# Kernel optimization log

Hardware: AMD Instinct MI355X
Metric: run time of the kernel (lower is better)

The kernel has to match this reference:

```python
import jax, jax.numpy as jnp
import numpy as np

L, H, NH, NKV, HD, I, V, B, S = 18, 640, 4, 1, 256, 2048, 32768, 1, 1024
WINDOW = 512
EPS = 1e-6
THETA_G = 1000000.0
THETA_L = 10000.0


def _rms(x, w):
    # Gemma RMSNorm: x / rms(x) * (1 + w)
    var = jnp.mean(jnp.square(x), axis=-1, keepdims=True)
    return x * jax.lax.rsqrt(var + EPS) * (1.0 + w)


def _rope_tables(theta):
    inv = 1.0 / (theta ** (jnp.arange(0, HD, 2, dtype=jnp.float32) / HD))
    f = jnp.arange(S, dtype=jnp.float32)[:, None] * inv[None, :]
    emb = jnp.concatenate([f, f], axis=-1)  # [S, HD]
    return jnp.cos(emb), jnp.sin(emb)


def _rope(x, cos, sin):
    # x: [B, S, n, HD]
    x1, x2 = jnp.split(x, 2, axis=-1)
    rot = jnp.concatenate([-x2, x1], axis=-1)
    return x * cos[None, :, None, :] + rot * sin[None, :, None, :]


def setup_inputs() -> dict:
    key = jax.random.key(0)
    ks = jax.random.split(key, 16)
    r = lambda k, sh: jax.random.normal(k, sh, jnp.float32) * 0.02
    return {
        'input_ids': jax.random.randint(ks[0], (B, S), 0, V, jnp.int32),
        'is_full': jnp.array([(i + 1) % 6 == 0 for i in range(L)]),
        'embed': r(ks[1], (V, H)),
        'wq': r(ks[2], (L, H, NH * HD)),
        'wk': r(ks[3], (L, H, NKV * HD)),
        'wv': r(ks[4], (L, H, NKV * HD)),
        'wo': r(ks[5], (L, NH * HD, H)),
        'qn': jnp.zeros((L, HD)), 'kn': jnp.zeros((L, HD)),
        'ln1': jnp.zeros((L, H)), 'ln2': jnp.zeros((L, H)),
        'ln3': jnp.zeros((L, H)), 'ln4': jnp.zeros((L, H)),
        'wg': r(ks[6], (L, H, I)), 'wu': r(ks[7], (L, H, I)),
        'wd': r(ks[8], (L, I, H)),
        'norm_w': jnp.zeros((H,)),
    }


def _forward(embed, wq, wk, wv, wo, qn, kn, ln1, ln2, ln3, ln4, wg, wu, wd,
             norm_w, input_ids, is_full):
    cos_g, sin_g = _rope_tables(THETA_G)
    cos_l, sin_l = _rope_tables(THETA_L)
    pos = jnp.arange(S)
    causal = pos[:, None] >= pos[None, :]
    sliding = causal & ((pos[:, None] - pos[None, :]) < WINDOW)
    scale = HD ** -0.5
    grp = NH // NKV

    h = embed[input_ids] * jnp.asarray(H ** 0.5, embed.dtype)  # [B,S,H]

    def body(h, xs):
        (wq_, wk_, wv_, wo_, qn_, kn_, l1, l2, l3, l4, wg_, wu_, wd_, full) = xs
        cos = jnp.where(full, cos_g, cos_l)
        sin = jnp.where(full, sin_g, sin_l)
        mask = jnp.where(full, causal, sliding)
        x = _rms(h, l1)
        q = (x @ wq_).reshape(B, S, NH, HD)
        k = (x @ wk_).reshape(B, S, NKV, HD)
        v = (x @ wv_).reshape(B, S, NKV, HD)
        q = _rope(_rms(q, qn_), cos, sin)
        k = _rope(_rms(k, kn_), cos, sin)
        qg = q.reshape(B, S, NKV, grp, HD)
        scores = jnp.einsum('bqngd,bsnd->bngqs', qg, k) * scale
        scores = jnp.where(mask[None, None, None], scores, -1e30)
        attn = jax.nn.softmax(scores, axis=-1)
        o = jnp.einsum('bngqs,bsnd->bqngd', attn, v).reshape(B, S, NH * HD)
        h = h + _rms(o @ wo_, l2)               # post_attention_layernorm then residual
        x = _rms(h, l3)                          # pre_feedforward_layernorm
        mlp = (jax.nn.gelu(x @ wg_, approximate=True) * (x @ wu_)) @ wd_  # GeGLU
        h = h + _rms(mlp, l4)                    # post_feedforward_layernorm then residual
        return h, None

    h, _ = jax.lax.scan(body, h, (wq, wk, wv, wo, qn, kn, ln1, ln2, ln3, ln4, wg, wu, wd, is_full))
    h = _rms(h, norm_w)
    # lm_head tied to embed_tokens; final_logit_softcapping = 0.0 (disabled)
    return jnp.einsum('bsh,vh->bsv', h, embed)


def reference(input_ids, is_full, embed, wq, wk, wv, wo, qn, kn,
              ln1, ln2, ln3, ln4, wg, wu, wd, norm_w):
    return _forward(embed, wq, wk, wv, wo, qn, kn, ln1, ln2, ln3, ln4,
                    wg, wu, wd, norm_w, input_ids, is_full)
```

## Files before the change

### kernel.cpp

```cpp
#include <hip/hip_runtime.h>


typedef unsigned short u16;
typedef __attribute__((ext_vector_type(4))) float f32x4;
typedef __attribute__((ext_vector_type(8))) short bf16x8;

#define DEV static __device__ __forceinline__
#define BIGN (1 << 30)

DEV u16 f2bf(float f) {
  union { float f; unsigned u; } x; x.f = f;
  unsigned r = x.u + 0x7fffu + ((x.u >> 16) & 1u);
  return (u16)(r >> 16);
}

#define GLOAD16(gp, lp) __builtin_amdgcn_global_load_lds( \
    (const __attribute__((address_space(1))) void*)(gp), \
    (__attribute__((address_space(3))) void*)(lp), 16, 0, 0)

DEV float blockSum(float v, float* red) {
#pragma unroll
  for (int o = 32; o; o >>= 1) v += __shfl_down(v, o);
  int lane = threadIdx.x & 63, wid = threadIdx.x >> 6;
  if (lane == 0) red[wid] = v;
  __syncthreads();
  float s = red[0] + red[1] + red[2] + red[3];
  __syncthreads();
  return s;
}

DEV float blockMax(float v, float* red) {
#pragma unroll
  for (int o = 32; o; o >>= 1) v = fmaxf(v, __shfl_down(v, o));
  int lane = threadIdx.x & 63, wid = threadIdx.x >> 6;
  if (lane == 0) red[wid] = v;
  __syncthreads();
  float s = fmaxf(fmaxf(red[0], red[1]), fmaxf(red[2], red[3]));
  __syncthreads();
  return s;
}

DEV void cstore(float* C, size_t i, float v) { C[i] = v; }
DEV void cstore(u16* C, size_t i, float v) { C[i] = f2bf(v); }

template <typename CT, int GEGLU, int BMODE>
__global__ __launch_bounds__(256) void gemm_nt(
    const u16* __restrict__ A, int lda, long sA,
    const void* __restrict__ B0v, int ldb0,
    const void* __restrict__ B1v, int ldb1,
    const void* __restrict__ B2v, int ldb2,
    int ns1, int ns2,
    CT* __restrict__ C, int ldc, long sC,
    int K, float alpha, int kmode, int nshift, int ksplit) {
  __shared__ __align__(16) u16 As[2 * 128 * 64];
  __shared__ __align__(16) u16 Bs[2 * 128 * 64];
  const int m0 = blockIdx.y * 128;
  int n0;
  if (nshift == -1) n0 = blockIdx.x * 128;
  else if (nshift == -2) { n0 = blockIdx.x * 128; if (n0 > m0) return; }
  else { n0 = m0 - nshift + blockIdx.x * 128; if (n0 < 0) return; }
  int klo = 0, khi = K;
  if (kmode == 1) { klo = m0 - 512; if (klo < 0) klo = 0; khi = m0 + 128; if (khi > K) khi = K; }
  else if (kmode == 2) { khi = m0 + 128; if (khi > K) khi = K; }
  else if (kmode == 3) { int kl = K / ksplit; klo = blockIdx.z * kl; khi = klo + kl; }
  A += (long)blockIdx.z * sA;

  const int t = threadIdx.x;
  const int l = t & 63, w = t >> 6;
  const int wr = w >> 1, wc = w & 1;
  const int lr = l & 15, lk = l >> 4;
  const int axr = lr & 7;
  const int srow = t >> 3;
  const int scolx = ((t & 7) ^ (srow & 7)) << 3;
  const u16* Ag = A + (size_t)(m0 + srow) * lda + scolx;
  const int nsteps = (khi - klo) >> 6;

  auto stageA = [&](int db, int k0) {
    u16* al = As + db * 8192 + w * 512;
#pragma unroll
    for (int p = 0; p < 4; ++p)
      GLOAD16(Ag + k0 + (size_t)(32 * p) * lda, al + p * 2048);
  };

  const u16* Bg16 = nullptr;
  const float* Bp = nullptr; int bldb = 0, bcol = 0, krow0 = 0;
  f32x4 fb[8];
  if constexpr (BMODE == 0) {
    Bg16 = (const u16*)B0v + (size_t)(n0 + srow) * ldb0 + scolx;
  } else if constexpr (BMODE == 1) {
    int rv = n0 + (l & 31) * 4;
    if (GEGLU) {
      int half = (rv >> 4) & 1;
      Bp = (const float*)(half ? B1v : B0v);
      bldb = half ? ldb1 : ldb0;
      bcol = (rv >> 5) * 16 + (rv & 15);
    } else if (rv >= ns2) { Bp = (const float*)B2v; bldb = ldb2; bcol = rv - ns2; }
    else if (rv >= ns1)   { Bp = (const float*)B1v; bldb = ldb1; bcol = rv - ns1; }
    else                  { Bp = (const float*)B0v; bldb = ldb0; bcol = rv; }
    krow0 = w * 16 + (l >> 5) * 8;
  } else {
    Bp = (const float*)B0v;
  }

  auto stageB0 = [&](int db, int k0) {
    u16* bl = Bs + db * 8192 + w * 512;
#pragma unroll
    for (int p = 0; p < 4; ++p)
      GLOAD16(Bg16 + k0 + (size_t)(32 * p) * ldb0, bl + p * 2048);
  };
  auto loadB = [&](int k0) {
    if constexpr (BMODE == 1) {
#pragma unroll
      for (int j = 0; j < 8; ++j)
        fb[j] = *(const f32x4*)&Bp[(size_t)(k0 + krow0 + j) * bldb + bcol];
    } else if constexpr (BMODE == 2) {
#pragma unroll
      for (int p = 0; p < 4; ++p)
#pragma unroll
        for (int q = 0; q < 2; ++q)
          fb[p * 2 + q] = *(const f32x4*)&Bp[(size_t)(n0 + srow + 32 * p) * ldb0 +
                                             k0 + (((t & 7) ^ (srow & 7)) << 3) + q * 4];
    }
  };
  auto writeB = [&](int db) {
    if constexpr (BMODE == 1) {
      int kb = w * 2 + (l >> 5);
#pragma unroll
      for (int e = 0; e < 4; ++e) {
        int row = (l & 31) * 4 + e;
        u16 tmp[8];
#pragma unroll
        for (int j = 0; j < 8; ++j) tmp[j] = f2bf(fb[j][e]);
        *(int4*)&Bs[db * 8192 + row * 64 + ((kb ^ (row & 7)) << 3)] = *(int4*)tmp;
      }
    } else if constexpr (BMODE == 2) {
#pragma unroll
      for (int p = 0; p < 4; ++p) {
        u16 tmp[8];
#pragma unroll
        for (int j = 0; j < 8; ++j) tmp[j] = f2bf(fb[p * 2 + j / 4][j & 3]);
        *(int4*)&Bs[db * 8192 + (srow + 32 * p) * 64 + ((t & 7) << 3)] = *(int4*)tmp;
      }
    }
  };

  f32x4 acc[4][4] = {};
  auto compute = [&](int db) {
    const u16* Ab = As + db * 8192;
    const u16* Bb = Bs + db * 8192;
    bf16x8 af[2][4], bfr[2][4];
#pragma unroll
    for (int kk = 0; kk < 2; ++kk)
#pragma unroll
      for (int i = 0; i < 4; ++i) {
        af[kk][i]  = *(const bf16x8*)&Ab[(wr * 64 + i * 16 + lr) * 64 + (((kk * 4 + lk) ^ axr) << 3)];
        bfr[kk][i] = *(const bf16x8*)&Bb[(wc * 64 + i * 16 + lr) * 64 + (((kk * 4 + lk) ^ axr) << 3)];
      }
#pragma unroll
    for (int kk = 0; kk < 2; ++kk)
#pragma unroll
      for (int mi = 0; mi < 4; ++mi)
#pragma unroll
        for (int ni = 0; ni < 4; ++ni)
          acc[mi][ni] = __builtin_amdgcn_mfma_f32_16x16x32_bf16(af[kk][mi], bfr[kk][ni], acc[mi][ni], 0, 0, 0);
  };

  if constexpr (BMODE == 0) {
    stageA(0, klo); stageB0(0, klo);
    for (int s = 0; s < nsteps; ++s) {
      __syncthreads();
      const int db = s & 1;
      if (s + 1 < nsteps) { stageA(db ^ 1, klo + (s + 1) * 64); stageB0(db ^ 1, klo + (s + 1) * 64); }
      compute(db);
    }
  } else {
    loadB(klo); stageA(0, klo);
    for (int s = 0; s < nsteps; ++s) {
      const int db = s & 1;
      writeB(db);
      if (s + 1 < nsteps) loadB(klo + (s + 1) * 64);
      __syncthreads();
      if (s + 1 < nsteps) stageA(db ^ 1, klo + (s + 1) * 64);
      compute(db);
    }
  }

  C += (long)blockIdx.z * sC;
  if (GEGLU) {
#pragma unroll
    for (int mi = 0; mi < 4; ++mi) {
      int row = m0 + wr * 64 + mi * 16 + lk * 4;
#pragma unroll
      for (int np = 0; np < 2; ++np) {
        int col = (n0 + wc * 64) / 2 + np * 16 + lr;
#pragma unroll
        for (int j = 0; j < 4; ++j) {
          float g = acc[mi][2 * np][j], u = acc[mi][2 * np + 1][j];
          float z = 0.7978845608028654f * (g + 0.044715f * g * g * g);
          float th = 2.0f / (1.0f + __expf(-2.0f * z)) - 1.0f;
          cstore(C, (size_t)(row + j) * ldc + col, 0.5f * g * (1.0f + th) * u);
        }
      }
    }
  } else {
#pragma unroll
    for (int mi = 0; mi < 4; ++mi) {
      int row = m0 + wr * 64 + mi * 16 + lk * 4;
#pragma unroll
      for (int ni = 0; ni < 4; ++ni) {
        int col = n0 + wc * 64 + ni * 16 + lr;
#pragma unroll
        for (int j = 0; j < 4; ++j)
          cstore(C, (size_t)(row + j) * ldc + col, acc[mi][ni][j] * alpha);
      }
    }
  }
}

__global__ void gather_rms_kernel(const int* __restrict__ ids, const float* __restrict__ embed,
                                  const float* __restrict__ w, float* __restrict__ h,
                                  u16* __restrict__ x) {
  __shared__ float red[8];
  const int s = blockIdx.x, t = threadIdx.x;
  const float* src = embed + (size_t)ids[s] * 640;
  const float scale = sqrtf(640.0f);
  float hv[3];
  float ss = 0.0f;
#pragma unroll
  for (int i = 0; i < 3; ++i) {
    int c = t + i * 256;
    float v = (c < 640) ? src[c] * scale : 0.0f;
    hv[i] = v; ss += v * v;
  }
  ss = blockSum(ss, red);
  const float sc = rsqrtf(ss * (1.0f / 640.0f) + 1e-6f);
#pragma unroll
  for (int i = 0; i < 3; ++i) {
    int c = t + i * 256;
    if (c < 640) {
      h[(size_t)s * 640 + c] = hv[i];
      x[(size_t)s * 640 + c] = f2bf(hv[i] * sc * (1.0f + w[c]));
    }
  }
}

__global__ void fused_add_norm(float* __restrict__ h, const float* __restrict__ t1,
                               int nsl, const float* __restrict__ wa,
                               const float* __restrict__ wn, u16* __restrict__ xout) {
  __shared__ float red[8];
  const int row = blockIdx.x, t = threadIdx.x;
  float ts[3], hv[3];
  float ss = 0.0f;
#pragma unroll
  for (int i = 0; i < 3; ++i) {
    int c = t + i * 256;
    float v = 0.0f;
    if (c < 640) {
      v = t1[(size_t)row * 640 + c];
      for (int z = 1; z < nsl; ++z) v += t1[(size_t)z * 655360 + (size_t)row * 640 + c];
    }
    ts[i] = v; ss += v * v;
  }
  ss = blockSum(ss, red);
  const float s1 = rsqrtf(ss * (1.0f / 640.0f) + 1e-6f);
  float ss2 = 0.0f;
#pragma unroll
  for (int i = 0; i < 3; ++i) {
    int c = t + i * 256;
    float v = 0.0f;
    if (c < 640) v = h[(size_t)row * 640 + c] + ts[i] * s1 * (1.0f + wa[c]);
    hv[i] = v; ss2 += v * v;
  }
  ss2 = blockSum(ss2, red);
  const float s2 = rsqrtf(ss2 * (1.0f / 640.0f) + 1e-6f);
#pragma unroll
  for (int i = 0; i < 3; ++i) {
    int c = t + i * 256;
    if (c < 640) {
      h[(size_t)row * 640 + c] = hv[i];
      xout[(size_t)row * 640 + c] = f2bf(hv[i] * s2 * (1.0f + wn[c]));
    }
  }
}

__global__ void rope_tables_kernel(float* cg, float* sg, float* cl, float* sl) {
  int s = blockIdx.x, t = threadIdx.x;
  float e = -(float)t * (1.0f / 128.0f);
  float ag = (float)s * expf(e * logf(1000000.0f));
  float al = (float)s * expf(e * logf(10000.0f));
  cg[s * 128 + t] = cosf(ag); sg[s * 128 + t] = sinf(ag);
  cl[s * 128 + t] = cosf(al); sl[s * 128 + t] = sinf(al);
}

__global__ void rope_fused(const float* __restrict__ qkvf, const float* __restrict__ qn,
                           const float* __restrict__ kn, u16* __restrict__ qb,
                           u16* __restrict__ kb, u16* __restrict__ vt,
                           const float* __restrict__ ct, const float* __restrict__ st) {
  __shared__ float red[8];
  __shared__ float sh[256];
  const int s = blockIdx.x, hh = blockIdx.y, t = threadIdx.x;
  const long SL = (long)1024 * 1536;
  if (hh == 5) {
    long i = (size_t)s * 1536 + 1280 + t;
    vt[(size_t)t * 1024 + s] = f2bf(qkvf[i] + qkvf[i + SL]);
    return;
  }
  long i = (size_t)s * 1536 + hh * 256 + t;
  const float* nw = (hh == 4) ? kn : qn;
  float x = qkvf[i] + qkvf[i + SL];
  float ss = blockSum(x * x, red);
  float n = x * rsqrtf(ss * (1.0f / 256.0f) + 1e-6f) * (1.0f + nw[t]);
  sh[t] = n;
  __syncthreads();
  float cosv = ct[s * 128 + (t & 127)];
  float sinv = st[s * 128 + (t & 127)];
  float partner = (t < 128) ? -sh[t + 128] : sh[t - 128];
  u16 r = f2bf(n * cosv + partner * sinv);
  if (hh == 4) kb[(size_t)s * 256 + t] = r;
  else qb[((size_t)hh * 1024 + s) * 256 + t] = r;
}

__global__ void softmax_kernel(const float* __restrict__ sc, u16* __restrict__ P, int mode) {
  __shared__ float red[8];
  const int i = blockIdx.x, hh = blockIdx.y, t = threadIdx.x;
  const float* row = sc + ((size_t)hh * 1024 + i) * 1024;
  u16* prow = P + ((size_t)hh * 1024 + i) * 1024;
  const int m0 = i & ~127;
  int lo = 0, wlo = 0;
  if (mode) {
    lo = i - 511; if (lo < 0) lo = 0;
    wlo = m0 - 512; if (wlo < 0) wlo = 0;
  }
  const int whi = m0 + 127;
  float m = -1e30f;
  for (int j = lo + t; j <= i; j += 256) m = fmaxf(m, row[j]);
  m = blockMax(m, red);
  float sum = 0.0f;
  for (int j = lo + t; j <= i; j += 256) sum += __expf(row[j] - m);
  sum = blockSum(sum, red);
  float inv = 1.0f / sum;
  for (int j = wlo + t; j <= whi; j += 256) {
    float v = (j >= lo && j <= i) ? __expf(row[j] - m) * inv : 0.0f;
    prow[j] = f2bf(v);
  }
}

extern "C" void kernel_launch(void* const* d_in, const int* in_sizes, int n_in,
                              void* d_out, int out_size, void* d_ws, size_t ws_size,
                              hipStream_t stream) {
  (void)in_sizes; (void)n_in; (void)out_size; (void)ws_size;
  const int*   ids   = (const int*)d_in[0];
  const float* embed = (const float*)d_in[2];
  const float* wq    = (const float*)d_in[3];
  const float* wk    = (const float*)d_in[4];
  const float* wv    = (const float*)d_in[5];
  const float* wo    = (const float*)d_in[6];
  const float* qn    = (const float*)d_in[7];
  const float* kn    = (const float*)d_in[8];
  const float* ln1   = (const float*)d_in[9];
  const float* ln2   = (const float*)d_in[10];
  const float* ln3   = (const float*)d_in[11];
  const float* ln4   = (const float*)d_in[12];
  const float* wg    = (const float*)d_in[13];
  const float* wu    = (const float*)d_in[14];
  const float* wd    = (const float*)d_in[15];
  const float* nw    = (const float*)d_in[16];
  float* out = (float*)d_out;

  const int S = 1024, H = 640, NH = 4, HD = 256, I = 2048, V = 32768;

  unsigned char* p = (unsigned char*)d_ws;
  auto alloc = [&](size_t b) { void* r = (void*)p; p += (b + 255) & ~(size_t)255; return r; };
  float* h     = (float*)alloc((size_t)S * H * 4);
  u16*   x     = (u16*)alloc((size_t)S * H * 2);
  float* qkvf  = (float*)alloc((size_t)2 * S * 1536 * 4);
  u16*   qb    = (u16*)alloc((size_t)NH * S * HD * 2);
  u16*   kb    = (u16*)alloc((size_t)S * HD * 2);
  u16*   vt    = (u16*)alloc((size_t)HD * S * 2);
  float* scp   = (float*)alloc((size_t)NH * S * S * 4);
  u16*   P     = (u16*)alloc((size_t)NH * S * S * 2);
  u16*   o     = (u16*)alloc((size_t)S * NH * HD * 2);
  float* t1    = (float*)alloc((size_t)4 * S * H * 4);
  u16*   mg    = (u16*)alloc((size_t)S * I * 2);
  u16*   hn    = (u16*)alloc((size_t)S * H * 2);
  float* cg    = (float*)alloc((size_t)S * 128 * 4);
  float* sg    = (float*)alloc((size_t)S * 128 * 4);
  float* cl    = (float*)alloc((size_t)S * 128 * 4);
  float* sl2   = (float*)alloc((size_t)S * 128 * 4);

  rope_tables_kernel<<<S, 128, 0, stream>>>(cg, sg, cl, sl2);
  gather_rms_kernel<<<S, 256, 0, stream>>>(ids, embed, ln1, h, x);

  for (int l = 0; l < 18; ++l) {
    bool full = ((l + 1) % 6) == 0;
    const float* wq_l = wq + (size_t)l * H * 1024;
    const float* wk_l = wk + (size_t)l * H * 256;
    const float* wv_l = wv + (size_t)l * H * 256;
    const float* wo_l = wo + (size_t)l * 1024 * H;
    const float* wg_l = wg + (size_t)l * H * I;
    const float* wu_l = wu + (size_t)l * H * I;
    const float* wd_l = wd + (size_t)l * I * H;

    gemm_nt<float, 0, 1><<<dim3(12, 8, 2), 256, 0, stream>>>(
        x, H, 0, wq_l, 1024, wk_l, 256, wv_l, 256, 1024, 1280,
        qkvf, 1536, (long)S * 1536, H, 1.0f, 3, -1, 2);
    rope_fused<<<dim3(S, 6), 256, 0, stream>>>(qkvf, qn + l * HD, kn + l * HD, qb, kb, vt,
                                               full ? cg : cl, full ? sg : sl2);
    if (full)
      gemm_nt<float, 0, 0><<<dim3(8, 8, NH), 256, 0, stream>>>(
          qb, HD, (long)S * HD, kb, HD, nullptr, 0, nullptr, 0, BIGN, BIGN,
          scp, S, (long)S * S, HD, 0.0625f, 0, -2, 1);
    else
      gemm_nt<float, 0, 0><<<dim3(5, 8, NH), 256, 0, stream>>>(
          qb, HD, (long)S * HD, kb, HD, nullptr, 0, nullptr, 0, BIGN, BIGN,
          scp, S, (long)S * S, HD, 0.0625f, 0, 512, 1);
    softmax_kernel<<<dim3(S, NH), 256, 0, stream>>>(scp, P, full ? 0 : 1);
    gemm_nt<u16, 0, 0><<<dim3(2, 8, NH), 256, 0, stream>>>(
        P, S, (long)S * S, vt, S, nullptr, 0, nullptr, 0, BIGN, BIGN,
        o, NH * HD, HD, S, 1.0f, full ? 2 : 1, -1, 1);
    gemm_nt<float, 0, 1><<<dim3(5, 8, 2), 256, 0, stream>>>(
        o, NH * HD, 0, wo_l, 640, nullptr, 0, nullptr, 0, BIGN, BIGN,
        t1, H, (long)S * H, NH * HD, 1.0f, 3, -1, 2);
    fused_add_norm<<<S, 256, 0, stream>>>(h, t1, 2, ln2 + l * H, ln3 + l * H, x);

    gemm_nt<u16, 1, 1><<<dim3(32, 8, 1), 256, 0, stream>>>(
        x, H, 0, wg_l, 2048, wu_l, 2048, nullptr, 0, BIGN, BIGN,
        mg, I, 0, H, 1.0f, 0, -1, 1);
    gemm_nt<float, 0, 1><<<dim3(5, 8, 4), 256, 0, stream>>>(
        mg, I, 0, wd_l, 640, nullptr, 0, nullptr, 0, BIGN, BIGN,
        t1, H, (long)S * H, I, 1.0f, 3, -1, 4);
    fused_add_norm<<<S, 256, 0, stream>>>(h, t1, 4, ln4 + l * H,
                                          (l == 17) ? nw : ln1 + (l + 1) * H,
                                          (l == 17) ? hn : x);
  }

  gemm_nt<float, 0, 2><<<dim3(V / 128, 8, 1), 256, 0, stream>>>(
      hn, H, 0, embed, H, nullptr, 0, nullptr, 0, BIGN, BIGN,
      out, V, 0, H, 1.0f, 0, -1, 1);
}
```

Before: 2.187 ms.

## Fuse softmax into PV matmul and swizzle block order for GeGLU/lm_head GEMMs

Removes the separate softmax kernel and bf16 P buffer. A new pv_fused kernel computes each row's max and sum from the fp32 scores, then forms normalized probabilities on the fly while feeding MFMA against V staged in LDS. It also adds a 1D grid mapping (nshift -3) that groups 8x8 tiles of M x N blocks for better L2 reuse in the GeGLU and lm_head GEMMs. The fused kernel reads the fp32 scores twice and runs only 64 blocks with single-buffered V loads, which may limit occupancy.

```diff
diff --git a/kernel.cpp b/kernel.cpp
--- a/kernel.cpp
+++ b/kernel.cpp
@@ -25,17 +25,6 @@
   if (lane == 0) red[wid] = v;
   __syncthreads();
   float s = red[0] + red[1] + red[2] + red[3];
-  __syncthreads();
-  return s;
-}
-
-DEV float blockMax(float v, float* red) {
-#pragma unroll
-  for (int o = 32; o; o >>= 1) v = fmaxf(v, __shfl_down(v, o));
-  int lane = threadIdx.x & 63, wid = threadIdx.x >> 6;
-  if (lane == 0) red[wid] = v;
-  __syncthreads();
-  float s = fmaxf(fmaxf(red[0], red[1]), fmaxf(red[2], red[3]));
   __syncthreads();
   return s;
 }
@@ -54,11 +43,17 @@
     int K, float alpha, int kmode, int nshift, int ksplit) {
   __shared__ __align__(16) u16 As[2 * 128 * 64];
   __shared__ __align__(16) u16 Bs[2 * 128 * 64];
-  const int m0 = blockIdx.y * 128;
-  int n0;
-  if (nshift == -1) n0 = blockIdx.x * 128;
-  else if (nshift == -2) { n0 = blockIdx.x * 128; if (n0 > m0) return; }
-  else { n0 = m0 - nshift + blockIdx.x * 128; if (n0 < 0) return; }
+  int m0, n0;
+  if (nshift == -3) {
+    int b = blockIdx.x;
+    m0 = ((b >> 3) & 7) * 128;
+    n0 = ((b >> 6) * 8 + (b & 7)) * 128;
+  } else {
+    m0 = blockIdx.y * 128;
+    if (nshift == -1) n0 = blockIdx.x * 128;
+    else if (nshift == -2) { n0 = blockIdx.x * 128; if (n0 > m0) return; }
+    else { n0 = m0 - nshift + blockIdx.x * 128; if (n0 < 0) return; }
+  }
   int klo = 0, khi = K;
   if (kmode == 1) { klo = m0 - 512; if (klo < 0) klo = 0; khi = m0 + 128; if (khi > K) khi = K; }
   else if (kmode == 2) { khi = m0 + 128; if (khi > K) khi = K; }
@@ -217,6 +212,115 @@
   }
 }
 
+__global__ __launch_bounds__(256) void pv_fused(
+    const float* __restrict__ scp, const u16* __restrict__ vt,
+    u16* __restrict__ o, int isfull) {
+  __shared__ __align__(16) u16 Vs[256 * 64];
+  __shared__ float mrow[64], invl[64];
+  const int m0 = blockIdx.x * 64, z = blockIdx.y;
+  const float* S_ = scp + (size_t)z * 1024 * 1024;
+  const int t = threadIdx.x;
+
+  {
+    int r = t >> 2, q = t & 3;
+    int row = m0 + r;
+    int lo = isfull ? 0 : (row - 511 > 0 ? row - 511 : 0);
+    const float* rp = S_ + (size_t)row * 1024;
+    float mx = -1e30f;
+    for (int j = lo + q; j <= row; j += 4) mx = fmaxf(mx, rp[j]);
+    mx = fmaxf(mx, __shfl_xor(mx, 1));
+    mx = fmaxf(mx, __shfl_xor(mx, 2));
+    float sum = 0.0f;
+    for (int j = lo + q; j <= row; j += 4) sum += __expf(rp[j] - mx);
+    sum += __shfl_xor(sum, 1);
+    sum += __shfl_xor(sum, 2);
+    if (q == 0) { mrow[r] = mx; invl[r] = 1.0f / sum; }
+  }
+  __syncthreads();
+
+  const int l = t & 63, w = t >> 6;
+  const int wr = w >> 1, wc = w & 1;
+  const int lr = l & 15, lk = l >> 4;
+  const int axr = lr & 7;
+  const int srow = t >> 3;
+  const int scolx = ((t & 7) ^ (srow & 7)) << 3;
+  const u16* Bg = vt + (size_t)srow * 1024 + scolx;
+  const int klo = isfull ? 0 : (m0 - 512 > 0 ? m0 - 512 : 0);
+  const int nsteps = (m0 + 64 - klo) >> 6;
+
+  int rowi[2]; float ms[2], ls[2];
+#pragma unroll
+  for (int i = 0; i < 2; ++i) {
+    rowi[i] = wr * 32 + i * 16 + lr;
+    ms[i] = mrow[rowi[i]];
+    ls[i] = invl[rowi[i]];
+  }
+
+  f32x4 acc[2][8] = {};
+  for (int s = 0; s < nsteps; ++s) {
+    const int k0 = klo + s * 64;
+    if (s) __syncthreads();
+    {
+      u16* bl = Vs + w * 512;
+#pragma unroll
+      for (int p = 0; p < 8; ++p)
+        GLOAD16(Bg + k0 + (size_t)(32 * p) * 1024, bl + p * 2048);
+    }
+    bf16x8 af[2][2];
+#pragma unroll
+    for (int kk = 0; kk < 2; ++kk)
+#pragma unroll
+      for (int i = 0; i < 2; ++i) {
+        int row = m0 + rowi[i];
+        int kb = k0 + kk * 32 + lk * 8;
+        const float* ap = S_ + (size_t)row * 1024 + kb;
+        float4 v0 = *(const float4*)ap;
+        float4 v1 = *(const float4*)(ap + 4);
+        float vv[8] = {v0.x, v0.y, v0.z, v0.w, v1.x, v1.y, v1.z, v1.w};
+        int lo = isfull ? 0 : row - 511;
+        u16 tmp[8];
+#pragma unroll
+        for (int e = 0; e < 8; ++e) {
+          int k = kb + e;
+          float pv = __expf(vv[e] - ms[i]) * ls[i];
+          tmp[e] = f2bf((k >= lo && k <= row) ? pv : 0.0f);
+        }
+        af[kk][i] = *(bf16x8*)tmp;
+      }
+    __syncthreads();
+#pragma unroll
+    for (int kk = 0; kk < 2; ++kk)
+#pragma unroll
+      for (int nh = 0; nh < 2; ++nh) {
+        bf16x8 bfr[4];
+#pragma unroll
+        for (int i = 0; i < 4; ++i)
+          bfr[i] = *(const bf16x8*)&Vs[(nh * 128 + wc * 64 + i * 16 + lr) * 64 +
+                                       (((kk * 4 + lk) ^ axr) << 3)];
+#pragma unroll
+        for (int mi = 0; mi < 2; ++mi)
+#pragma unroll
+          for (int ni = 0; ni < 4; ++ni)
+            acc[mi][nh * 4 + ni] = __builtin_amdgcn_mfma_f32_16x16x32_bf16(
+                af[kk][mi], bfr[ni], acc[mi][nh * 4 + ni], 0, 0, 0);
+      }
+  }
+
+#pragma unroll
+  for (int mi = 0; mi < 2; ++mi) {
+    int row = m0 + wr * 32 + mi * 16 + lk * 4;
+#pragma unroll
+    for (int nh = 0; nh < 2; ++nh)
+#pragma unroll
+      for (int ni = 0; ni < 4; ++ni) {
+        int col = z * 256 + nh * 128 + wc * 64 + ni * 16 + lr;
+#pragma unroll
+        for (int j = 0; j < 4; ++j)
+          o[(size_t)(row + j) * 1024 + col] = f2bf(acc[mi][nh * 4 + ni][j]);
+      }
+  }
+}
+
 __global__ void gather_rms_kernel(const int* __restrict__ ids, const float* __restrict__ embed,
                                   const float* __restrict__ w, float* __restrict__ h,
                                   u16* __restrict__ x) {
@@ -318,31 +422,6 @@
   u16 r = f2bf(n * cosv + partner * sinv);
   if (hh == 4) kb[(size_t)s * 256 + t] = r;
   else qb[((size_t)hh * 1024 + s) * 256 + t] = r;
-}
-
-__global__ void softmax_kernel(const float* __restrict__ sc, u16* __restrict__ P, int mode) {
-  __shared__ float red[8];
-  const int i = blockIdx.x, hh = blockIdx.y, t = threadIdx.x;
-  const float* row = sc + ((size_t)hh * 1024 + i) * 1024;
-  u16* prow = P + ((size_t)hh * 1024 + i) * 1024;
-  const int m0 = i & ~127;
-  int lo = 0, wlo = 0;
-  if (mode) {
-    lo = i - 511; if (lo < 0) lo = 0;
-    wlo = m0 - 512; if (wlo < 0) wlo = 0;
-  }
-  const int whi = m0 + 127;
-  float m = -1e30f;
-  for (int j = lo + t; j <= i; j += 256) m = fmaxf(m, row[j]);
-  m = blockMax(m, red);
-  float sum = 0.0f;
-  for (int j = lo + t; j <= i; j += 256) sum += __expf(row[j] - m);
-  sum = blockSum(sum, red);
-  float inv = 1.0f / sum;
-  for (int j = wlo + t; j <= whi; j += 256) {
-    float v = (j >= lo && j <= i) ? __expf(row[j] - m) * inv : 0.0f;
-    prow[j] = f2bf(v);
-  }
 }
 
 extern "C" void kernel_launch(void* const* d_in, const int* in_sizes, int n_in,
@@ -378,7 +457,6 @@
   u16*   kb    = (u16*)alloc((size_t)S * HD * 2);
   u16*   vt    = (u16*)alloc((size_t)HD * S * 2);
   float* scp   = (float*)alloc((size_t)NH * S * S * 4);
-  u16*   P     = (u16*)alloc((size_t)NH * S * S * 2);
   u16*   o     = (u16*)alloc((size_t)S * NH * HD * 2);
   float* t1    = (float*)alloc((size_t)4 * S * H * 4);
   u16*   mg    = (u16*)alloc((size_t)S * I * 2);
@@ -414,18 +492,15 @@
       gemm_nt<float, 0, 0><<<dim3(5, 8, NH), 256, 0, stream>>>(
           qb, HD, (long)S * HD, kb, HD, nullptr, 0, nullptr, 0, BIGN, BIGN,
           scp, S, (long)S * S, HD, 0.0625f, 0, 512, 1);
-    softmax_kernel<<<dim3(S, NH), 256, 0, stream>>>(scp, P, full ? 0 : 1);
-    gemm_nt<u16, 0, 0><<<dim3(2, 8, NH), 256, 0, stream>>>(
-        P, S, (long)S * S, vt, S, nullptr, 0, nullptr, 0, BIGN, BIGN,
-        o, NH * HD, HD, S, 1.0f, full ? 2 : 1, -1, 1);
+    pv_fused<<<dim3(16, NH), 256, 0, stream>>>(scp, vt, o, full ? 1 : 0);
     gemm_nt<float, 0, 1><<<dim3(5, 8, 2), 256, 0, stream>>>(
         o, NH * HD, 0, wo_l, 640, nullptr, 0, nullptr, 0, BIGN, BIGN,
         t1, H, (long)S * H, NH * HD, 1.0f, 3, -1, 2);
     fused_add_norm<<<S, 256, 0, stream>>>(h, t1, 2, ln2 + l * H, ln3 + l * H, x);
 
-    gemm_nt<u16, 1, 1><<<dim3(32, 8, 1), 256, 0, stream>>>(
+    gemm_nt<u16, 1, 1><<<dim3(256, 1, 1), 256, 0, stream>>>(
         x, H, 0, wg_l, 2048, wu_l, 2048, nullptr, 0, BIGN, BIGN,
-        mg, I, 0, H, 1.0f, 0, -1, 1);
+        mg, I, 0, H, 1.0f, 0, -3, 1);
     gemm_nt<float, 0, 1><<<dim3(5, 8, 4), 256, 0, stream>>>(
         mg, I, 0, wd_l, 640, nullptr, 0, nullptr, 0, BIGN, BIGN,
         t1, H, (long)S * H, I, 1.0f, 3, -1, 4);
@@ -434,7 +509,7 @@
                                           (l == 17) ? hn : x);
   }
 
-  gemm_nt<float, 0, 2><<<dim3(V / 128, 8, 1), 256, 0, stream>>>(
+  gemm_nt<float, 0, 2><<<dim3(2048, 1, 1), 256, 0, stream>>>(
       hn, H, 0, embed, H, nullptr, 0, nullptr, 0, BIGN, BIGN,
-      out, V, 0, H, 1.0f, 0, -1, 1);
-}
+      out, V, 0, H, 1.0f, 0, -3, 1);
+}
```

After: 2.890 ms. 1.32x slower.

## Pre-convert embedding to bf16, drop split-K on QKV, read V directly from projection

Applied to the files above, without the earlier changes.

The tied embedding is converted to bf16 once up front, so the LM-head GEMM can use async LDS loads (BMODE 0) instead of converting fp32 per tile. That GEMM also gets a swizzled 1D block mapping that groups blocks sharing embedding columns. The QKV projection drops split-K, which removes the partial-sum buffer and the add in rope. The separate V-transpose pass is removed, and the PV GEMM reads V in fp32 straight from the QKV buffer through the k-major convert path. The trade-offs are lower QKV parallelism, an extra conversion pass over the embedding, and fp32 V reads repeated for each head.

```diff
diff --git a/kernel.cpp b/kernel.cpp
--- a/kernel.cpp
+++ b/kernel.cpp
@@ -54,11 +54,17 @@
     int K, float alpha, int kmode, int nshift, int ksplit) {
   __shared__ __align__(16) u16 As[2 * 128 * 64];
   __shared__ __align__(16) u16 Bs[2 * 128 * 64];
-  const int m0 = blockIdx.y * 128;
-  int n0;
-  if (nshift == -1) n0 = blockIdx.x * 128;
-  else if (nshift == -2) { n0 = blockIdx.x * 128; if (n0 > m0) return; }
-  else { n0 = m0 - nshift + blockIdx.x * 128; if (n0 < 0) return; }
+  int m0, n0;
+  if (nshift == -3) {
+    int b = blockIdx.x;
+    m0 = ((b >> 3) & 7) * 128;
+    n0 = ((b >> 6) * 8 + (b & 7)) * 128;
+  } else {
+    m0 = blockIdx.y * 128;
+    if (nshift == -1) n0 = blockIdx.x * 128;
+    else if (nshift == -2) { n0 = blockIdx.x * 128; if (n0 > m0) return; }
+    else { n0 = m0 - nshift + blockIdx.x * 128; if (n0 < 0) return; }
+  }
   int klo = 0, khi = K;
   if (kmode == 1) { klo = m0 - 512; if (klo < 0) klo = 0; khi = m0 + 128; if (khi > K) khi = K; }
   else if (kmode == 2) { khi = m0 + 128; if (khi > K) khi = K; }
@@ -87,7 +93,7 @@
   f32x4 fb[8];
   if constexpr (BMODE == 0) {
     Bg16 = (const u16*)B0v + (size_t)(n0 + srow) * ldb0 + scolx;
-  } else if constexpr (BMODE == 1) {
+  } else {
     int rv = n0 + (l & 31) * 4;
     if (GEGLU) {
       int half = (rv >> 4) & 1;
@@ -98,8 +104,6 @@
     else if (rv >= ns1)   { Bp = (const float*)B1v; bldb = ldb1; bcol = rv - ns1; }
     else                  { Bp = (const float*)B0v; bldb = ldb0; bcol = rv; }
     krow0 = w * 16 + (l >> 5) * 8;
-  } else {
-    Bp = (const float*)B0v;
   }
 
   auto stageB0 = [&](int db, int k0) {
@@ -109,38 +113,19 @@
       GLOAD16(Bg16 + k0 + (size_t)(32 * p) * ldb0, bl + p * 2048);
   };
   auto loadB = [&](int k0) {
-    if constexpr (BMODE == 1) {
-#pragma unroll
-      for (int j = 0; j < 8; ++j)
-        fb[j] = *(const f32x4*)&Bp[(size_t)(k0 + krow0 + j) * bldb + bcol];
-    } else if constexpr (BMODE == 2) {
-#pragma unroll
-      for (int p = 0; p < 4; ++p)
-#pragma unroll
-        for (int q = 0; q < 2; ++q)
-          fb[p * 2 + q] = *(const f32x4*)&Bp[(size_t)(n0 + srow + 32 * p) * ldb0 +
-                                             k0 + (((t & 7) ^ (srow & 7)) << 3) + q * 4];
-    }
+#pragma unroll
+    for (int j = 0; j < 8; ++j)
+      fb[j] = *(const f32x4*)&Bp[(size_t)(k0 + krow0 + j) * bldb + bcol];
   };
   auto writeB = [&](int db) {
-    if constexpr (BMODE == 1) {
-      int kb = w * 2 + (l >> 5);
-#pragma unroll
-      for (int e = 0; e < 4; ++e) {
-        int row = (l & 31) * 4 + e;
-        u16 tmp[8];
-#pragma unroll
-        for (int j = 0; j < 8; ++j) tmp[j] = f2bf(fb[j][e]);
-        *(int4*)&Bs[db * 8192 + row * 64 + ((kb ^ (row & 7)) << 3)] = *(int4*)tmp;
-      }
-    } else if constexpr (BMODE == 2) {
-#pragma unroll
-      for (int p = 0; p < 4; ++p) {
-        u16 tmp[8];
-#pragma unroll
-        for (int j = 0; j < 8; ++j) tmp[j] = f2bf(fb[p * 2 + j / 4][j & 3]);
-        *(int4*)&Bs[db * 8192 + (srow + 32 * p) * 64 + ((t & 7) << 3)] = *(int4*)tmp;
-      }
+    int kb = w * 2 + (l >> 5);
+#pragma unroll
+    for (int e = 0; e < 4; ++e) {
+      int row = (l & 31) * 4 + e;
+      u16 tmp[8];
+#pragma unroll
+      for (int j = 0; j < 8; ++j) tmp[j] = f2bf(fb[j][e]);
+      *(int4*)&Bs[db * 8192 + row * 64 + ((kb ^ (row & 7)) << 3)] = *(int4*)tmp;
     }
   };
 
@@ -217,6 +202,14 @@
   }
 }
 
+__global__ void conv_bf16_kernel(const float* __restrict__ in, u16* __restrict__ out, long n4) {
+  for (long i = (long)blockIdx.x * blockDim.x + threadIdx.x; i < n4; i += (long)gridDim.x * blockDim.x) {
+    float4 v = ((const float4*)in)[i];
+    ushort4 o4 = { f2bf(v.x), f2bf(v.y), f2bf(v.z), f2bf(v.w) };
+    ((ushort4*)out)[i] = o4;
+  }
+}
+
 __global__ void gather_rms_kernel(const int* __restrict__ ids, const float* __restrict__ embed,
                                   const float* __restrict__ w, float* __restrict__ h,
                                   u16* __restrict__ x) {
@@ -294,20 +287,14 @@
 
 __global__ void rope_fused(const float* __restrict__ qkvf, const float* __restrict__ qn,
                            const float* __restrict__ kn, u16* __restrict__ qb,
-                           u16* __restrict__ kb, u16* __restrict__ vt,
+                           u16* __restrict__ kb,
                            const float* __restrict__ ct, const float* __restrict__ st) {
   __shared__ float red[8];
   __shared__ float sh[256];
   const int s = blockIdx.x, hh = blockIdx.y, t = threadIdx.x;
-  const long SL = (long)1024 * 1536;
-  if (hh == 5) {
-    long i = (size_t)s * 1536 + 1280 + t;
-    vt[(size_t)t * 1024 + s] = f2bf(qkvf[i] + qkvf[i + SL]);
-    return;
-  }
-  long i = (size_t)s * 1536 + hh * 256 + t;
+  const float* src = qkvf + (size_t)s * 1536 + hh * 256;
   const float* nw = (hh == 4) ? kn : qn;
-  float x = qkvf[i] + qkvf[i + SL];
+  float x = src[t];
   float ss = blockSum(x * x, red);
   float n = x * rsqrtf(ss * (1.0f / 256.0f) + 1e-6f) * (1.0f + nw[t]);
   sh[t] = n;
@@ -371,12 +358,12 @@
 
   unsigned char* p = (unsigned char*)d_ws;
   auto alloc = [&](size_t b) { void* r = (void*)p; p += (b + 255) & ~(size_t)255; return r; };
+  u16*   embT  = (u16*)alloc((size_t)V * H * 2);
   float* h     = (float*)alloc((size_t)S * H * 4);
   u16*   x     = (u16*)alloc((size_t)S * H * 2);
-  float* qkvf  = (float*)alloc((size_t)2 * S * 1536 * 4);
+  float* qkvf  = (float*)alloc((size_t)S * 1536 * 4);
   u16*   qb    = (u16*)alloc((size_t)NH * S * HD * 2);
   u16*   kb    = (u16*)alloc((size_t)S * HD * 2);
-  u16*   vt    = (u16*)alloc((size_t)HD * S * 2);
   float* scp   = (float*)alloc((size_t)NH * S * S * 4);
   u16*   P     = (u16*)alloc((size_t)NH * S * S * 2);
   u16*   o     = (u16*)alloc((size_t)S * NH * HD * 2);
@@ -389,6 +376,7 @@
   float* sl2   = (float*)alloc((size_t)S * 128 * 4);
 
   rope_tables_kernel<<<S, 128, 0, stream>>>(cg, sg, cl, sl2);
+  conv_bf16_kernel<<<2048, 256, 0, stream>>>(embed, embT, (long)V * H / 4);
   gather_rms_kernel<<<S, 256, 0, stream>>>(ids, embed, ln1, h, x);
 
   for (int l = 0; l < 18; ++l) {
@@ -401,10 +389,10 @@
     const float* wu_l = wu + (size_t)l * H * I;
     const float* wd_l = wd + (size_t)l * I * H;
 
-    gemm_nt<float, 0, 1><<<dim3(12, 8, 2), 256, 0, stream>>>(
+    gemm_nt<float, 0, 1><<<dim3(12, 8, 1), 256, 0, stream>>>(
         x, H, 0, wq_l, 1024, wk_l, 256, wv_l, 256, 1024, 1280,
-        qkvf, 1536, (long)S * 1536, H, 1.0f, 3, -1, 2);
-    rope_fused<<<dim3(S, 6), 256, 0, stream>>>(qkvf, qn + l * HD, kn + l * HD, qb, kb, vt,
+        qkvf, 1536, 0, H, 1.0f, 0, -1, 1);
+    rope_fused<<<dim3(S, 5), 256, 0, stream>>>(qkvf, qn + l * HD, kn + l * HD, qb, kb,
                                                full ? cg : cl, full ? sg : sl2);
     if (full)
       gemm_nt<float, 0, 0><<<dim3(8, 8, NH), 256, 0, stream>>>(
@@ -415,8 +403,8 @@
           qb, HD, (long)S * HD, kb, HD, nullptr, 0, nullptr, 0, BIGN, BIGN,
           scp, S, (long)S * S, HD, 0.0625f, 0, 512, 1);
     softmax_kernel<<<dim3(S, NH), 256, 0, stream>>>(scp, P, full ? 0 : 1);
-    gemm_nt<u16, 0, 0><<<dim3(2, 8, NH), 256, 0, stream>>>(
-        P, S, (long)S * S, vt, S, nullptr, 0, nullptr, 0, BIGN, BIGN,
+    gemm_nt<u16, 0, 1><<<dim3(2, 8, NH), 256, 0, stream>>>(
+        P, S, (long)S * S, qkvf + 1280, 1536, nullptr, 0, nullptr, 0, BIGN, BIGN,
         o, NH * HD, HD, S, 1.0f, full ? 2 : 1, -1, 1);
     gemm_nt<float, 0, 1><<<dim3(5, 8, 2), 256, 0, stream>>>(
         o, NH * HD, 0, wo_l, 640, nullptr, 0, nullptr, 0, BIGN, BIGN,
@@ -434,7 +422,7 @@
                                           (l == 17) ? hn : x);
   }
 
-  gemm_nt<float, 0, 2><<<dim3(V / 128, 8, 1), 256, 0, stream>>>(
-      hn, H, 0, embed, H, nullptr, 0, nullptr, 0, BIGN, BIGN,
-      out, V, 0, H, 1.0f, 0, -1, 1);
-}
+  gemm_nt<float, 0, 0><<<dim3(2048, 1, 1), 256, 0, stream>>>(
+      hn, H, 0, embT, H, nullptr, 0, nullptr, 0, BIGN, BIGN,
+      out, V, 0, H, 1.0f, 0, -3, 1);
+}
```

Result: slower. 2.380 ms (+8.8%).
